# Optimization experiments

Measured on AMD Instinct MI355X. Metric: run time of the kernel, lower is better.

Reference implementation:

```python
import jax, jax.numpy as jnp
import numpy as np

NUM_TAGS = 19
START_ID = 17  # lbl_to_id['START_LBL']
PAD_ID = 18    # lbl_to_id['PAD_LBL']
NEG = -1000.0


def setup_inputs() -> dict:
    key = jax.random.key(0)
    k1, k2, k3 = jax.random.split(key, 3)
    B, L = 512, 2048
    P = jax.random.normal(k1, (B, L, NUM_TAGS), dtype=jnp.float32)
    T = jax.random.normal(k2, (NUM_TAGS, NUM_TAGS), dtype=jnp.float32)
    # contiguous-prefix valid mask, lengths in [1, L]
    lengths = jax.random.randint(k3, (B,), 1, L + 1)
    mask = jnp.arange(L)[None, :] < lengths[:, None]  # [B, L] bool
    return {"P": P, "T": T, "mask": mask}


def _viterbi_forward(P, T, mask):
    # P: [B, L, K] emissions; T[j, k] = score of transition prev=k -> cur=j
    B, L, K = P.shape
    DP0 = jnp.full((B, K), NEG, dtype=P.dtype).at[:, START_ID].set(0.0)

    def step(DP, xs):
        emit, m = xs  # emit: [B, K], m: [B] bool
        scores = DP[:, None, :] + T[None, :, :]        # [B, cur, prev]
        best = scores.max(axis=-1)                      # [B, K]
        arg = scores.argmax(axis=-1).astype(jnp.int32)  # [B, K] backpointers
        new_DP = best + emit
        DP = jnp.where(m[:, None], new_DP, DP)          # frozen past sequence end
        return DP, arg

    DP, choice = jax.lax.scan(
        step, DP0, (jnp.swapaxes(P, 0, 1), jnp.swapaxes(mask, 0, 1))
    )  # choice: [L, B, K]
    DP = DP + T[PAD_ID][None, :]  # transition into PAD at the end
    return DP, choice


def reference(P, T, mask):
    B, L, K = P.shape
    DP, choice = _viterbi_forward(P, T, mask)
    last = DP.argmax(axis=-1).astype(jnp.int32)          # [B] best final tag
    lengths = mask.sum(axis=-1).astype(jnp.int32)        # [B]
    bidx = jnp.arange(B)

    def back(c, t):
        # path[t] = choice[t+1][path[t+1]] for t < len-1; path[len-1] = last
        nxt = choice[jnp.minimum(t + 1, L - 1), bidx, c]  # [B]
        new_c = jnp.where(t < lengths - 1, nxt, c)
        out = jnp.where(t < lengths, new_c, -1)           # -1 pads beyond length
        return new_c, out

    _, outs = jax.lax.scan(back, last, jnp.arange(L - 1, -1, -1))  # [L, B]
    path = jnp.flip(jnp.swapaxes(outs, 0, 1), axis=1)  # [B, L], decoded tags
    return path
```

## Files before the change

### kernel.cpp

```cpp
#include <hip/hip_runtime.h>

#define Bn 512
#define Ln 2048
#define Kn 19
#define NEGV (-1000.0f)
#define START_IDn 17
#define PAD_IDn 18
#define SEG 64
#define PBYTES 79691776u


#define DP_CORE(BASE)                                                          \
    float4 q0 = *(const float4*)((BASE) + 0);                                  \
    float4 q1 = *(const float4*)((BASE) + 4);                                  \
    float4 q2 = *(const float4*)((BASE) + 8);                                  \
    float4 q3 = *(const float4*)((BASE) + 12);                                 \
    float4 q4 = *(const float4*)((BASE) + 16);            \
    float cand[Kn];                                                            \
    cand[0]  = q0.x + Trow[0];  cand[1]  = q0.y + Trow[1];                     \
    cand[2]  = q0.z + Trow[2];  cand[3]  = q0.w + Trow[3];                     \
    cand[4]  = q1.x + Trow[4];  cand[5]  = q1.y + Trow[5];                     \
    cand[6]  = q1.z + Trow[6];  cand[7]  = q1.w + Trow[7];                     \
    cand[8]  = q2.x + Trow[8];  cand[9]  = q2.y + Trow[9];                     \
    cand[10] = q2.z + Trow[10]; cand[11] = q2.w + Trow[11];                    \
    cand[12] = q3.x + Trow[12]; cand[13] = q3.y + Trow[13];                    \
    cand[14] = q3.z + Trow[14]; cand[15] = q3.w + Trow[15];                    \
    cand[16] = q4.x + Trow[16]; cand[17] = q4.y + Trow[17];                    \
    cand[18] = q4.z + Trow[18];                                                \
    float m0 = fmaxf(fmaxf(cand[0],  cand[1]),  cand[2]);                      \
    float m1 = fmaxf(fmaxf(cand[3],  cand[4]),  cand[5]);                      \
    float m2 = fmaxf(fmaxf(cand[6],  cand[7]),  cand[8]);                      \
    float m3 = fmaxf(fmaxf(cand[9],  cand[10]), cand[11]);                     \
    float m4 = fmaxf(fmaxf(cand[12], cand[13]), cand[14]);                     \
    float m5 = fmaxf(fmaxf(cand[15], cand[16]), cand[17]);                     \
    float n0 = fmaxf(fmaxf(m0, m1), m2);                                       \
    float n1 = fmaxf(fmaxf(m3, m4), cand[18]);                                 \
    float best = fmaxf(fmaxf(n0, n1), m5);

__global__ __launch_bounds__(64, 1) void crf_fwd(
    const float* __restrict__ P, const float* __restrict__ T,
    const int* __restrict__ mask, float* __restrict__ dpck,
    float* __restrict__ dpfin, int* __restrict__ lens)
{
    const int lane = threadIdx.x;
    const int half = lane >> 5;
    const int c = lane & 31;
    const int b = blockIdx.x * 2 + half;
    const int cc = (c < Kn) ? c : (Kn - 1);

    float Trow[Kn];
#pragma unroll
    for (int p = 0; p < Kn; ++p) Trow[p] = T[cc * Kn + p];

    const int* mrow = mask + (size_t)b * Ln;
    int sum = 0;
#pragma unroll
    for (int j = 0; j < Ln / 128; ++j) {
        int4 v = *(const int4*)(mrow + j * 128 + c * 4);
        sum += v.x + v.y + v.z + v.w;
    }
#pragma unroll
    for (int k = 1; k < 32; k <<= 1) sum += __shfl_xor(sum, k, 64);
    const int len = sum;
    if (c == 0) lens[b] = len;
    const int lenO = __shfl_xor(len, 32, 64);
    int maxlen = len > lenO ? len : lenO;
    int lmin = len < lenO ? len : lenO;
    lmin = __builtin_amdgcn_readfirstlane(lmin);
    int mlen = (maxlen + (SEG - 1)) & ~(SEG - 1);
    mlen = __builtin_amdgcn_readfirstlane(mlen);

    __shared__ float dp[2][32];
    __shared__ float ebuf[2][2][1280];

    float mydp = (c == START_IDn) ? 0.0f : NEGV;
    dp[half][c] = mydp;

    const unsigned bbyte = (unsigned)b * (Ln * Kn * 4u);
    const unsigned limit = PBYTES - 16;
    const char* Pc = (const char*)P;
    float4 r[10];

#define STAGE_LOAD(ci)                                                         \
    { unsigned base_ = bbyte + (unsigned)(ci) * 4864u + ((unsigned)c << 4);    \
      _Pragma("unroll")                                                        \
      for (int i_ = 0; i_ < 10; ++i_) {                                        \
          unsigned o_ = base_ + (unsigned)i_ * 512u;                           \
          if (o_ > limit) o_ = limit;                                          \
          r[i_] = *(const float4*)(Pc + o_);                                   \
      } }
#define STAGE_WRITE(nb)                                                        \
    { float* d_ = &ebuf[nb][half][(unsigned)c << 2];                           \
      _Pragma("unroll")                                                        \
      for (int i_ = 0; i_ < 10; ++i_) *(float4*)(d_ + i_ * 128) = r[i_]; }

    int buf = 0;
    STAGE_LOAD(0);
    STAGE_WRITE(0);

    for (int t0 = 0; t0 < mlen; t0 += SEG) {
        if (c < Kn)
            dpck[((unsigned)b * 32u + (unsigned)(t0 >> 6)) * (unsigned)Kn + (unsigned)c] = mydp;
        STAGE_LOAD((t0 >> 6) + 1);
        const float* ebl = &ebuf[buf][half][0];

        if (t0 + SEG <= lmin) {
            for (int tt = 0; tt < SEG; tt += 8) {
#pragma unroll
                for (int u = 0; u < 8; ++u) {
                    const float e = ebl[(tt + u) * Kn + cc];
                    const float* base_ = &dp[half][0];
                    DP_CORE(base_)
                    mydp = best + e;
                    dp[half][c] = mydp;
                }
            }
        } else {
            for (int tt = 0; tt < SEG; tt += 8) {
#pragma unroll
                for (int u = 0; u < 8; ++u) {
                    const int t = t0 + tt + u;
                    const float e = ebl[(tt + u) * Kn + cc];
                    const float* base_ = &dp[half][0];
                    DP_CORE(base_)
                    float nd = best + e;
                    mydp = (t < len) ? nd : mydp;
                    dp[half][c] = mydp;
                }
            }
        }
        STAGE_WRITE(buf ^ 1);
        buf ^= 1;
    }
    if (c < Kn) dpfin[b * Kn + c] = mydp;
#undef STAGE_LOAD
#undef STAGE_WRITE
}

__global__ __launch_bounds__(256) void crf_rec(
    const float* __restrict__ P, const float* __restrict__ T,
    const float* __restrict__ dpck, const int* __restrict__ lens,
    unsigned char* __restrict__ choice)
{
    const int tid = threadIdx.x;
    const int halfid = tid >> 5;
    const int c = tid & 31;
    const int cc = (c < Kn) ? c : (Kn - 1);
    const int task = blockIdx.x * 8 + halfid;
    const int b = task >> 5;
    const int seg = task & 31;
    const int t0 = seg * SEG;
    const int len = lens[b];
    if (t0 >= len) return;

    __shared__ float dp[8][32];
    __shared__ __align__(16) unsigned char cbuf[8][SEG * Kn];

    float Trow[Kn];
#pragma unroll
    for (int p = 0; p < Kn; ++p) Trow[p] = T[cc * Kn + p];

    float mydp = (c < Kn) ? dpck[((unsigned)b * 32u + (unsigned)seg) * (unsigned)Kn + (unsigned)c]
                          : NEGV;
    dp[halfid][c] = mydp;

    const float* prow = P + (size_t)b * Ln * Kn + (size_t)t0 * Kn;

    float eb[8];
#pragma unroll
    for (int u = 0; u < 8; ++u) eb[u] = prow[u * Kn + cc];

    for (int tt = 0; tt < SEG; tt += 8) {
#pragma unroll
        for (int u = 0; u < 8; ++u) {
            const int t = t0 + tt + u;
            const float e = eb[u];
            const float* base_ = &dp[halfid][0];
            DP_CORE(base_)
            float nd = best + e;
            mydp = (t < len) ? nd : mydp;
            dp[halfid][c] = mydp;

            int arg = Kn - 1;
#pragma unroll
            for (int p = Kn - 2; p >= 0; --p)
                arg = (cand[p] == best) ? p : arg;
            if (c < Kn) cbuf[halfid][(tt + u) * Kn + c] = (unsigned char)arg;

            int tn = tt + u + 8;
            int tloc = (t0 + tn < Ln) ? tn : (Ln - 1 - t0);
            eb[u] = prow[tloc * Kn + cc];
        }
    }
    {
        const int4* s = (const int4*)&cbuf[halfid][0];
        int4* d = (int4*)(choice + (size_t)b * Ln * Kn + (size_t)t0 * Kn);
        for (int i = c; i < (SEG * Kn) / 16; i += 32) d[i] = s[i];
    }
}

__global__ __launch_bounds__(384, 1) void crf_bwd(
    const float* __restrict__ T, const unsigned char* __restrict__ choice,
    const float* __restrict__ dpfin, const int* __restrict__ lens,
    int* __restrict__ out)
{
    __shared__ unsigned char comp[Ln * Kn];
    __shared__ int vchain[17];
    __shared__ int s_last, s_len;

    const int b = blockIdx.x;
    const int tid = threadIdx.x;

    {
        const int4* src = (const int4*)(choice + (size_t)b * Ln * Kn);
        int4* dst = (int4*)comp;
        for (int i = tid; i < (Ln * Kn) / 16; i += 384) dst[i] = src[i];
    }
    if (tid == 0) {
        s_len = lens[b];
        float bestv = dpfin[b * Kn + 0] + T[PAD_IDn * Kn + 0];
        int bl = 0;
        for (int ci = 1; ci < Kn; ++ci) {
            float v = dpfin[b * Kn + ci] + T[PAD_IDn * Kn + ci];
            if (v > bestv) { bestv = v; bl = ci; }
        }
        s_last = bl;
    }
    __syncthreads();
    const int len = s_len;

    {
        const int wv = tid >> 6;
        const int lane = tid & 63;
        const int ch = wv * 3 + lane / Kn;
        const int c = lane % Kn;
        if (lane < 3 * Kn && ch < 16) {
            int cur = c;
            const int tb = ch * 128 + 127;
            for (int i = 0; i < 128; ++i) {
                const int t = tb - i;
                int nv = comp[t * Kn + cur];
                cur = (t < len) ? nv : cur;
                comp[t * Kn + c] = cur;
            }
        }
    }
    __syncthreads();

    if (tid == 0) {
        int v = s_last;
        vchain[16] = v;
        for (int ch = 15; ch >= 0; --ch) {
            v = comp[ch * 128 * Kn + v];
            vchain[ch] = v;
        }
    }
    __syncthreads();

    const int last = s_last;
    int* orow = out + (size_t)b * Ln;
    for (int t = tid; t < Ln; t += 384) {
        int val;
        if (t >= len) {
            val = -1;
        } else if (t == Ln - 1) {
            val = last;
        } else {
            const int tp = t + 1;
            const int vc = vchain[(tp >> 7) + 1];
            val = comp[tp * Kn + vc];
        }
        orow[t] = val;
    }
}

extern "C" void kernel_launch(void* const* d_in, const int* in_sizes, int n_in,
                              void* d_out, int out_size, void* d_ws, size_t ws_size,
                              hipStream_t stream)
{
    const float* P    = (const float*)d_in[0];
    const float* T    = (const float*)d_in[1];
    const int*   mask = (const int*)d_in[2];
    int* out = (int*)d_out;

    const size_t choice_bytes = (size_t)Bn * Ln * Kn;
    unsigned char* choice = (unsigned char*)d_ws;
    float* dpfin = (float*)((char*)d_ws + choice_bytes);
    int* lens = (int*)((char*)d_ws + choice_bytes + (size_t)Bn * Kn * 4);

    float* dpck = (float*)((char*)d_out + 2 * 1024 * 1024);

    crf_fwd<<<Bn / 2, 64, 0, stream>>>(P, T, mask, dpck, dpfin, lens);
    crf_rec<<<(Bn * 32) / 8, 256, 0, stream>>>(P, T, dpck, lens, choice);
    crf_bwd<<<Bn, 384, 0, stream>>>(T, choice, dpfin, lens, out);
}
```

Before: 400.3 us.

## Use one batch row per wave with readlane DP broadcast in forward pass

Reassigns the forward Viterbi kernel from two rows per wave (half-waves) to one row per wave, doubling the grid. The per-step DP exchange through shared memory is replaced by 19 readlane broadcasts, removing the LDS store/load round trip from the serial dependency chain. Each row now iterates only to its own length instead of the pair's maximum. Trade-off: half the lanes per wave are idle and more waves are launched, and readlane serialization may add its own latency.

```diff
diff --git a/kernel.cpp b/kernel.cpp
--- a/kernel.cpp
+++ b/kernel.cpp
@@ -37,16 +37,32 @@
     float n1 = fmaxf(fmaxf(m3, m4), cand[18]);                                 \
     float best = fmaxf(fmaxf(n0, n1), m5);
 
+#define FWD_CORE()                                                             \
+    float cand[Kn];                                                            \
+    _Pragma("unroll")                                                          \
+    for (int p_ = 0; p_ < Kn; ++p_) {                                          \
+        float s_ = __uint_as_float(                                            \
+            __builtin_amdgcn_readlane(__float_as_uint(mydp), p_));             \
+        cand[p_] = s_ + Trow[p_];                                              \
+    }                                                                          \
+    float m0 = fmaxf(fmaxf(cand[0],  cand[1]),  cand[2]);                      \
+    float m1 = fmaxf(fmaxf(cand[3],  cand[4]),  cand[5]);                      \
+    float m2 = fmaxf(fmaxf(cand[6],  cand[7]),  cand[8]);                      \
+    float m3 = fmaxf(fmaxf(cand[9],  cand[10]), cand[11]);                     \
+    float m4 = fmaxf(fmaxf(cand[12], cand[13]), cand[14]);                     \
+    float m5 = fmaxf(fmaxf(cand[15], cand[16]), cand[17]);                     \
+    float n0 = fmaxf(fmaxf(m0, m1), m2);                                       \
+    float n1 = fmaxf(fmaxf(m3, m4), cand[18]);                                 \
+    float best = fmaxf(fmaxf(n0, n1), m5);
+
 __global__ __launch_bounds__(64, 1) void crf_fwd(
     const float* __restrict__ P, const float* __restrict__ T,
     const int* __restrict__ mask, float* __restrict__ dpck,
     float* __restrict__ dpfin, int* __restrict__ lens)
 {
     const int lane = threadIdx.x;
-    const int half = lane >> 5;
-    const int c = lane & 31;
-    const int b = blockIdx.x * 2 + half;
-    const int cc = (c < Kn) ? c : (Kn - 1);
+    const int b = blockIdx.x;
+    const int cc = (lane < Kn) ? lane : (Kn - 1);
 
     float Trow[Kn];
 #pragma unroll
@@ -55,64 +71,55 @@
     const int* mrow = mask + (size_t)b * Ln;
     int sum = 0;
 #pragma unroll
-    for (int j = 0; j < Ln / 128; ++j) {
-        int4 v = *(const int4*)(mrow + j * 128 + c * 4);
+    for (int j = 0; j < Ln / 256; ++j) {
+        int4 v = *(const int4*)(mrow + j * 256 + lane * 4);
         sum += v.x + v.y + v.z + v.w;
     }
 #pragma unroll
-    for (int k = 1; k < 32; k <<= 1) sum += __shfl_xor(sum, k, 64);
-    const int len = sum;
-    if (c == 0) lens[b] = len;
-    const int lenO = __shfl_xor(len, 32, 64);
-    int maxlen = len > lenO ? len : lenO;
-    int lmin = len < lenO ? len : lenO;
-    lmin = __builtin_amdgcn_readfirstlane(lmin);
-    int mlen = (maxlen + (SEG - 1)) & ~(SEG - 1);
-    mlen = __builtin_amdgcn_readfirstlane(mlen);
-
-    __shared__ float dp[2][32];
-    __shared__ float ebuf[2][2][1280];
-
-    float mydp = (c == START_IDn) ? 0.0f : NEGV;
-    dp[half][c] = mydp;
+    for (int k = 1; k < 64; k <<= 1) sum += __shfl_xor(sum, k, 64);
+    int len = __builtin_amdgcn_readfirstlane(sum);
+    if (lane == 0) lens[b] = len;
+    const int mlen = (len + (SEG - 1)) & ~(SEG - 1);
+
+    __shared__ float ebuf[2][1280];
+
+    float mydp = (lane == START_IDn) ? 0.0f : NEGV;
 
     const unsigned bbyte = (unsigned)b * (Ln * Kn * 4u);
     const unsigned limit = PBYTES - 16;
     const char* Pc = (const char*)P;
-    float4 r[10];
+    float4 r[5];
 
 #define STAGE_LOAD(ci)                                                         \
-    { unsigned base_ = bbyte + (unsigned)(ci) * 4864u + ((unsigned)c << 4);    \
+    { unsigned base_ = bbyte + (unsigned)(ci) * 4864u + ((unsigned)lane << 4); \
       _Pragma("unroll")                                                        \
-      for (int i_ = 0; i_ < 10; ++i_) {                                        \
-          unsigned o_ = base_ + (unsigned)i_ * 512u;                           \
+      for (int i_ = 0; i_ < 5; ++i_) {                                         \
+          unsigned o_ = base_ + (unsigned)i_ * 1024u;                          \
           if (o_ > limit) o_ = limit;                                          \
           r[i_] = *(const float4*)(Pc + o_);                                   \
       } }
 #define STAGE_WRITE(nb)                                                        \
-    { float* d_ = &ebuf[nb][half][(unsigned)c << 2];                           \
+    { float* d_ = &ebuf[nb][(unsigned)lane << 2];                              \
       _Pragma("unroll")                                                        \
-      for (int i_ = 0; i_ < 10; ++i_) *(float4*)(d_ + i_ * 128) = r[i_]; }
+      for (int i_ = 0; i_ < 5; ++i_) *(float4*)(d_ + i_ * 256) = r[i_]; }
 
     int buf = 0;
     STAGE_LOAD(0);
     STAGE_WRITE(0);
 
     for (int t0 = 0; t0 < mlen; t0 += SEG) {
-        if (c < Kn)
-            dpck[((unsigned)b * 32u + (unsigned)(t0 >> 6)) * (unsigned)Kn + (unsigned)c] = mydp;
+        if (lane < Kn)
+            dpck[((unsigned)b * 32u + (unsigned)(t0 >> 6)) * (unsigned)Kn + (unsigned)lane] = mydp;
         STAGE_LOAD((t0 >> 6) + 1);
-        const float* ebl = &ebuf[buf][half][0];
-
-        if (t0 + SEG <= lmin) {
+        const float* ebl = &ebuf[buf][0];
+
+        if (t0 + SEG <= len) {
             for (int tt = 0; tt < SEG; tt += 8) {
 #pragma unroll
                 for (int u = 0; u < 8; ++u) {
                     const float e = ebl[(tt + u) * Kn + cc];
-                    const float* base_ = &dp[half][0];
-                    DP_CORE(base_)
+                    FWD_CORE()
                     mydp = best + e;
-                    dp[half][c] = mydp;
                 }
             }
         } else {
@@ -121,18 +128,16 @@
                 for (int u = 0; u < 8; ++u) {
                     const int t = t0 + tt + u;
                     const float e = ebl[(tt + u) * Kn + cc];
-                    const float* base_ = &dp[half][0];
-                    DP_CORE(base_)
+                    FWD_CORE()
                     float nd = best + e;
                     mydp = (t < len) ? nd : mydp;
-                    dp[half][c] = mydp;
                 }
             }
         }
         STAGE_WRITE(buf ^ 1);
         buf ^= 1;
     }
-    if (c < Kn) dpfin[b * Kn + c] = mydp;
+    if (lane < Kn) dpfin[b * Kn + lane] = mydp;
 #undef STAGE_LOAD
 #undef STAGE_WRITE
 }
@@ -290,7 +295,7 @@
 
     float* dpck = (float*)((char*)d_out + 2 * 1024 * 1024);
 
-    crf_fwd<<<Bn / 2, 64, 0, stream>>>(P, T, mask, dpck, dpfin, lens);
+    crf_fwd<<<Bn, 64, 0, stream>>>(P, T, mask, dpck, dpfin, lens);
     crf_rec<<<(Bn * 32) / 8, 256, 0, stream>>>(P, T, dpck, lens, choice);
     crf_bwd<<<Bn, 384, 0, stream>>>(T, choice, dpfin, lens, out);
 }
```

New measurement: 476.4 us. 1.19x slower.

## Pack four sequences per wave in forward pass using DPP/swizzle cross-lane exchange

Applied to the files above, without the earlier changes.

The forward Viterbi kernel is restructured so each 16-lane group handles one sequence, with every lane owning one primary tag and lanes 0-2 also owning tags 16-18. Previous-step scores are exchanged through DPP row permutes and ds_swizzle instead of an LDS round-trip, and emissions are prefetched straight from global memory into registers eight steps ahead instead of being staged through LDS. This halves the number of forward blocks and shortens the per-step dependency chain. The cost is more instructions per step (two max trees per lane) and scattered, non-vectorized global loads of emissions.

```diff
diff --git a/kernel.cpp b/kernel.cpp
--- a/kernel.cpp
+++ b/kernel.cpp
@@ -37,104 +37,147 @@
     float n1 = fmaxf(fmaxf(m3, m4), cand[18]);                                 \
     float best = fmaxf(fmaxf(n0, n1), m5);
 
+#define DPPF(x, ctrl) (__int_as_float(__builtin_amdgcn_update_dpp(            \
+    __float_as_int(x), __float_as_int(x), (ctrl), 0xF, 0xF, false)))
+#define SWZF(x, off) (__int_as_float(__builtin_amdgcn_ds_swizzle(             \
+    __float_as_int(x), (off))))
+
+#define TREE19(RES, TT, GT)                                                    \
+    {                                                                          \
+      float d0 = v0 + TT[0],  d1 = v1 + TT[1],  d2 = v2 + TT[2];               \
+      float d3 = v3 + TT[3],  d4 = v4 + TT[4],  d5 = v5 + TT[5];               \
+      float d6 = v6 + TT[6],  d7 = v7 + TT[7],  d8 = v8 + TT[8];               \
+      float d9 = v9 + TT[9],  d10 = va + TT[10], d11 = vb + TT[11];            \
+      float d12 = vc + TT[12], d13 = vd + TT[13], d14 = ve + TT[14];           \
+      float d15 = vf + TT[15];                                                 \
+      float e16 = g0 + GT[0], e17 = g1 + GT[1], e18 = g2 + GT[2];              \
+      float m0 = fmaxf(fmaxf(d0, d1), d2);                                     \
+      float m1 = fmaxf(fmaxf(d3, d4), d5);                                     \
+      float m2 = fmaxf(fmaxf(d6, d7), d8);                                     \
+      float m3 = fmaxf(fmaxf(d9, d10), d11);                                   \
+      float m4 = fmaxf(fmaxf(d12, d13), d14);                                  \
+      float m5 = fmaxf(fmaxf(d15, e16), e17);                                  \
+      float n0 = fmaxf(fmaxf(m0, m1), m2);                                     \
+      float n1 = fmaxf(fmaxf(m3, m4), m5);                                     \
+      RES = fmaxf(fmaxf(n0, n1), e18);                                         \
+    }
+
+#define FSTEP(U, MASKED)                                                       \
+  {                                                                            \
+    const int t = t0 + tt + (U);                                               \
+    const float v0 = A;                                                        \
+    const float v1 = DPPF(A, 0xB1);                                            \
+    const float v2 = DPPF(A, 0x4E);                                            \
+    const float v3 = DPPF(A, 0x1B);                                            \
+    const float v7 = DPPF(A, 0x141);                                           \
+    const float v6 = DPPF(v7, 0xB1);                                           \
+    const float v5 = DPPF(v7, 0x4E);                                           \
+    const float v4 = DPPF(v7, 0x1B);                                           \
+    const float vf = DPPF(A, 0x140);                                           \
+    const float ve = DPPF(vf, 0xB1);                                           \
+    const float vd = DPPF(vf, 0x4E);                                           \
+    const float vc = DPPF(vf, 0x1B);                                           \
+    const float v8 = DPPF(vf, 0x141);                                          \
+    const float v9 = DPPF(v8, 0xB1);                                           \
+    const float va = DPPF(v8, 0x4E);                                           \
+    const float vb = DPPF(v8, 0x1B);                                           \
+    float bp, bs;                                                              \
+    TREE19(bp, Tp, Gp)                                                         \
+    TREE19(bs, Ts, Gs)                                                         \
+    const float nd  = bp + eb[(U)];                                            \
+    const float nd2 = bs + eb2[(U)];                                           \
+    if (MASKED) {                                                              \
+      A   = (t < len) ? nd  : A;                                               \
+      sec = (t < len) ? nd2 : sec;                                             \
+    } else {                                                                   \
+      A   = nd;                                                                \
+      sec = nd2;                                                               \
+    }                                                                          \
+    g0 = SWZF(sec, 0x10);                                                      \
+    g1 = SWZF(sec, 0x30);                                                      \
+    g2 = SWZF(sec, 0x50);                                                      \
+    int tn = t + 8;                                                            \
+    tn = (tn < Ln) ? tn : (Ln - 1);                                            \
+    eb[(U)]  = prow[tn * Kn + jr];                                             \
+    eb2[(U)] = prow[tn * Kn + o2];                                             \
+  }
+
 __global__ __launch_bounds__(64, 1) void crf_fwd(
     const float* __restrict__ P, const float* __restrict__ T,
     const int* __restrict__ mask, float* __restrict__ dpck,
     float* __restrict__ dpfin, int* __restrict__ lens)
 {
     const int lane = threadIdx.x;
-    const int half = lane >> 5;
-    const int c = lane & 31;
-    const int b = blockIdx.x * 2 + half;
-    const int cc = (c < Kn) ? c : (Kn - 1);
-
-    float Trow[Kn];
-#pragma unroll
-    for (int p = 0; p < Kn; ++p) Trow[p] = T[cc * Kn + p];
+    const int jr = lane & 15;
+    const int row = lane >> 4;
+    const int b = blockIdx.x * 4 + row;
+    const int o2 = 16 + ((jr < 3) ? jr : 2);
+
+    float Tp[16], Ts[16], Gp[3], Gs[3];
+#pragma unroll
+    for (int m = 0; m < 16; ++m) {
+        Tp[m] = T[jr * Kn + (jr ^ m)];
+        Ts[m] = T[o2 * Kn + (jr ^ m)];
+    }
+#pragma unroll
+    for (int i = 0; i < 3; ++i) {
+        Gp[i] = T[jr * Kn + 16 + i];
+        Gs[i] = T[o2 * Kn + 16 + i];
+    }
 
     const int* mrow = mask + (size_t)b * Ln;
     int sum = 0;
 #pragma unroll
-    for (int j = 0; j < Ln / 128; ++j) {
-        int4 v = *(const int4*)(mrow + j * 128 + c * 4);
+    for (int j2 = 0; j2 < 32; ++j2) {
+        int4 v = *(const int4*)(mrow + j2 * 64 + jr * 4);
         sum += v.x + v.y + v.z + v.w;
     }
-#pragma unroll
-    for (int k = 1; k < 32; k <<= 1) sum += __shfl_xor(sum, k, 64);
+    sum += __shfl_xor(sum, 1, 64);
+    sum += __shfl_xor(sum, 2, 64);
+    sum += __shfl_xor(sum, 4, 64);
+    sum += __shfl_xor(sum, 8, 64);
     const int len = sum;
-    if (c == 0) lens[b] = len;
-    const int lenO = __shfl_xor(len, 32, 64);
-    int maxlen = len > lenO ? len : lenO;
-    int lmin = len < lenO ? len : lenO;
-    lmin = __builtin_amdgcn_readfirstlane(lmin);
-    int mlen = (maxlen + (SEG - 1)) & ~(SEG - 1);
-    mlen = __builtin_amdgcn_readfirstlane(mlen);
-
-    __shared__ float dp[2][32];
-    __shared__ float ebuf[2][2][1280];
-
-    float mydp = (c == START_IDn) ? 0.0f : NEGV;
-    dp[half][c] = mydp;
-
-    const unsigned bbyte = (unsigned)b * (Ln * Kn * 4u);
-    const unsigned limit = PBYTES - 16;
-    const char* Pc = (const char*)P;
-    float4 r[10];
-
-#define STAGE_LOAD(ci)                                                         \
-    { unsigned base_ = bbyte + (unsigned)(ci) * 4864u + ((unsigned)c << 4);    \
-      _Pragma("unroll")                                                        \
-      for (int i_ = 0; i_ < 10; ++i_) {                                        \
-          unsigned o_ = base_ + (unsigned)i_ * 512u;                           \
-          if (o_ > limit) o_ = limit;                                          \
-          r[i_] = *(const float4*)(Pc + o_);                                   \
-      } }
-#define STAGE_WRITE(nb)                                                        \
-    { float* d_ = &ebuf[nb][half][(unsigned)c << 2];                           \
-      _Pragma("unroll")                                                        \
-      for (int i_ = 0; i_ < 10; ++i_) *(float4*)(d_ + i_ * 128) = r[i_]; }
-
-    int buf = 0;
-    STAGE_LOAD(0);
-    STAGE_WRITE(0);
+    if (jr == 0) lens[b] = len;
+    int lx = len, ln_ = len;
+    { int u16a = __shfl_xor(lx, 16, 64); lx = lx > u16a ? lx : u16a;
+      int u16b = __shfl_xor(ln_, 16, 64); ln_ = ln_ < u16b ? ln_ : u16b; }
+    { int u32a = __shfl_xor(lx, 32, 64); lx = lx > u32a ? lx : u32a;
+      int u32b = __shfl_xor(ln_, 32, 64); ln_ = ln_ < u32b ? ln_ : u32b; }
+    const int lmin = __builtin_amdgcn_readfirstlane(ln_);
+    const int mlen = (__builtin_amdgcn_readfirstlane(lx) + (SEG - 1)) & ~(SEG - 1);
+
+    float A = NEGV;
+    float sec = (jr == 1) ? 0.0f : NEGV;
+    float g0 = NEGV, g1 = 0.0f, g2 = NEGV;
+
+    const float* prow = P + (size_t)b * Ln * Kn;
+    float eb[8], eb2[8];
+#pragma unroll
+    for (int u = 0; u < 8; ++u) {
+        eb[u]  = prow[u * Kn + jr];
+        eb2[u] = prow[u * Kn + o2];
+    }
 
     for (int t0 = 0; t0 < mlen; t0 += SEG) {
-        if (c < Kn)
-            dpck[((unsigned)b * 32u + (unsigned)(t0 >> 6)) * (unsigned)Kn + (unsigned)c] = mydp;
-        STAGE_LOAD((t0 >> 6) + 1);
-        const float* ebl = &ebuf[buf][half][0];
-
+        {
+            const unsigned ck = ((unsigned)b * 32u + (unsigned)(t0 >> 6)) * (unsigned)Kn;
+            dpck[ck + (unsigned)jr] = A;
+            if (jr < 3) dpck[ck + 16u + (unsigned)jr] = sec;
+        }
         if (t0 + SEG <= lmin) {
             for (int tt = 0; tt < SEG; tt += 8) {
-#pragma unroll
-                for (int u = 0; u < 8; ++u) {
-                    const float e = ebl[(tt + u) * Kn + cc];
-                    const float* base_ = &dp[half][0];
-                    DP_CORE(base_)
-                    mydp = best + e;
-                    dp[half][c] = mydp;
-                }
+                FSTEP(0, 0) FSTEP(1, 0) FSTEP(2, 0) FSTEP(3, 0)
+                FSTEP(4, 0) FSTEP(5, 0) FSTEP(6, 0) FSTEP(7, 0)
             }
         } else {
             for (int tt = 0; tt < SEG; tt += 8) {
-#pragma unroll
-                for (int u = 0; u < 8; ++u) {
-                    const int t = t0 + tt + u;
-                    const float e = ebl[(tt + u) * Kn + cc];
-                    const float* base_ = &dp[half][0];
-                    DP_CORE(base_)
-                    float nd = best + e;
-                    mydp = (t < len) ? nd : mydp;
-                    dp[half][c] = mydp;
-                }
+                FSTEP(0, 1) FSTEP(1, 1) FSTEP(2, 1) FSTEP(3, 1)
+                FSTEP(4, 1) FSTEP(5, 1) FSTEP(6, 1) FSTEP(7, 1)
             }
         }
-        STAGE_WRITE(buf ^ 1);
-        buf ^= 1;
-    }
-    if (c < Kn) dpfin[b * Kn + c] = mydp;
-#undef STAGE_LOAD
-#undef STAGE_WRITE
+    }
+    dpfin[b * Kn + jr] = A;
+    if (jr < 3) dpfin[b * Kn + 16 + jr] = sec;
 }
 
 __global__ __launch_bounds__(256) void crf_rec(
@@ -290,7 +333,7 @@
 
     float* dpck = (float*)((char*)d_out + 2 * 1024 * 1024);
 
-    crf_fwd<<<Bn / 2, 64, 0, stream>>>(P, T, mask, dpck, dpfin, lens);
+    crf_fwd<<<Bn / 4, 64, 0, stream>>>(P, T, mask, dpck, dpfin, lens);
     crf_rec<<<(Bn * 32) / 8, 256, 0, stream>>>(P, T, dpck, lens, choice);
     crf_bwd<<<Bn, 384, 0, stream>>>(T, choice, dpfin, lens, out);
 }
```

Measured after the change: 624.5 us. +56.0%, slower.

## Fuse forward and recompute kernels with producer-consumer wavefronts in one block

Applied to the files above, without the earlier changes.

Merges the forward max-plus scan kernel and the segment recompute/backpointer kernel into one 192-thread block. One wavefront runs the forward DP for two sequences and publishes per-segment checkpoints through shared memory with a flag. Two consumer wavefronts spin-wait on that flag and recompute backpointers for finished segments while the forward pass continues. This removes the global checkpoint round-trip and a kernel launch, and overlaps backpointer work with the serial forward scan. In exchange, the recompute runs on only 2 wavefronts per pair of sequences instead of a wide separate grid, and the spin-wait adds contention on the forward wavefront.

```diff
diff --git a/kernel.cpp b/kernel.cpp
--- a/kernel.cpp
+++ b/kernel.cpp
@@ -37,49 +37,62 @@
     float n1 = fmaxf(fmaxf(m3, m4), cand[18]);                                 \
     float best = fmaxf(fmaxf(n0, n1), m5);
 
-__global__ __launch_bounds__(64, 1) void crf_fwd(
+__global__ __launch_bounds__(192, 1) void crf_fused(
     const float* __restrict__ P, const float* __restrict__ T,
-    const int* __restrict__ mask, float* __restrict__ dpck,
-    float* __restrict__ dpfin, int* __restrict__ lens)
+    const int* __restrict__ mask, float* __restrict__ dpfin,
+    int* __restrict__ lens, unsigned char* __restrict__ choice)
 {
-    const int lane = threadIdx.x;
-    const int half = lane >> 5;
-    const int c = lane & 31;
-    const int b = blockIdx.x * 2 + half;
-    const int cc = (c < Kn) ? c : (Kn - 1);
-
-    float Trow[Kn];
-#pragma unroll
-    for (int p = 0; p < Kn; ++p) Trow[p] = T[cc * Kn + p];
-
-    const int* mrow = mask + (size_t)b * Ln;
-    int sum = 0;
-#pragma unroll
-    for (int j = 0; j < Ln / 128; ++j) {
-        int4 v = *(const int4*)(mrow + j * 128 + c * 4);
-        sum += v.x + v.y + v.z + v.w;
-    }
-#pragma unroll
-    for (int k = 1; k < 32; k <<= 1) sum += __shfl_xor(sum, k, 64);
-    const int len = sum;
-    if (c == 0) lens[b] = len;
-    const int lenO = __shfl_xor(len, 32, 64);
-    int maxlen = len > lenO ? len : lenO;
-    int lmin = len < lenO ? len : lenO;
-    lmin = __builtin_amdgcn_readfirstlane(lmin);
-    int mlen = (maxlen + (SEG - 1)) & ~(SEG - 1);
-    mlen = __builtin_amdgcn_readfirstlane(mlen);
+    const int tid = threadIdx.x;
+    const int w = tid >> 6;
 
     __shared__ float dp[2][32];
     __shared__ float ebuf[2][2][1280];
-
-    float mydp = (c == START_IDn) ? 0.0f : NEGV;
-    dp[half][c] = mydp;
-
-    const unsigned bbyte = (unsigned)b * (Ln * Kn * 4u);
-    const unsigned limit = PBYTES - 16;
-    const char* Pc = (const char*)P;
-    float4 r[10];
+    __shared__ float ckbuf[2][32][20];
+    __shared__ int   s_len2[2];
+    __shared__ int   seg_done[2];
+    __shared__ float rdp[2][2][32];
+    __shared__ __align__(16) unsigned char rcbuf[2][2][1280];
+
+    if (tid < 2) *(volatile int*)&seg_done[tid] = 0;
+    __syncthreads();
+
+    if (w == 0) {
+        __builtin_amdgcn_s_setprio(1);
+        const int lane = tid;
+        const int half = lane >> 5;
+        const int c = lane & 31;
+        const int b = blockIdx.x * 2 + half;
+        const int cc = (c < Kn) ? c : (Kn - 1);
+
+        float Trow[Kn];
+#pragma unroll
+        for (int p = 0; p < Kn; ++p) Trow[p] = T[cc * Kn + p];
+
+        const int* mrow = mask + (size_t)b * Ln;
+        int sum = 0;
+#pragma unroll
+        for (int j = 0; j < Ln / 128; ++j) {
+            int4 v = *(const int4*)(mrow + j * 128 + c * 4);
+            sum += v.x + v.y + v.z + v.w;
+        }
+#pragma unroll
+        for (int k = 1; k < 32; k <<= 1) sum += __shfl_xor(sum, k, 64);
+        const int len = sum;
+        if (c == 0) { lens[b] = len; s_len2[half] = len; }
+        const int lenO = __shfl_xor(len, 32, 64);
+        int maxlen = len > lenO ? len : lenO;
+        int lmin = len < lenO ? len : lenO;
+        lmin = __builtin_amdgcn_readfirstlane(lmin);
+        int mlen = (maxlen + (SEG - 1)) & ~(SEG - 1);
+        mlen = __builtin_amdgcn_readfirstlane(mlen);
+
+        float mydp = (c == START_IDn) ? 0.0f : NEGV;
+        dp[half][c] = mydp;
+
+        const unsigned bbyte = (unsigned)b * (Ln * Kn * 4u);
+        const unsigned limit = PBYTES - 16;
+        const char* Pc = (const char*)P;
+        float4 r[10];
 
 #define STAGE_LOAD(ci)                                                         \
     { unsigned base_ = bbyte + (unsigned)(ci) * 4864u + ((unsigned)c << 4);    \
@@ -94,108 +107,118 @@
       _Pragma("unroll")                                                        \
       for (int i_ = 0; i_ < 10; ++i_) *(float4*)(d_ + i_ * 128) = r[i_]; }
 
-    int buf = 0;
-    STAGE_LOAD(0);
-    STAGE_WRITE(0);
-
-    for (int t0 = 0; t0 < mlen; t0 += SEG) {
-        if (c < Kn)
-            dpck[((unsigned)b * 32u + (unsigned)(t0 >> 6)) * (unsigned)Kn + (unsigned)c] = mydp;
-        STAGE_LOAD((t0 >> 6) + 1);
-        const float* ebl = &ebuf[buf][half][0];
-
-        if (t0 + SEG <= lmin) {
-            for (int tt = 0; tt < SEG; tt += 8) {
-#pragma unroll
-                for (int u = 0; u < 8; ++u) {
-                    const float e = ebl[(tt + u) * Kn + cc];
-                    const float* base_ = &dp[half][0];
-                    DP_CORE(base_)
-                    mydp = best + e;
-                    dp[half][c] = mydp;
+        int buf = 0;
+        STAGE_LOAD(0);
+        STAGE_WRITE(0);
+
+        for (int t0 = 0; t0 < mlen; t0 += SEG) {
+            if (c < Kn) ckbuf[half][t0 >> 6][c] = mydp;
+            __threadfence_block();
+            __asm__ __volatile__("" ::: "memory");
+            if (c == 0) *(volatile int*)&seg_done[half] = (t0 >> 6) + 1;
+
+            STAGE_LOAD((t0 >> 6) + 1);
+            const float* ebl = &ebuf[buf][half][0];
+
+            if (t0 + SEG <= lmin) {
+                for (int tt = 0; tt < SEG; tt += 8) {
+#pragma unroll
+                    for (int u = 0; u < 8; ++u) {
+                        const float e = ebl[(tt + u) * Kn + cc];
+                        const float* base_ = &dp[half][0];
+                        DP_CORE(base_)
+                        mydp = best + e;
+                        dp[half][c] = mydp;
+                    }
                 }
-            }
-        } else {
-            for (int tt = 0; tt < SEG; tt += 8) {
-#pragma unroll
-                for (int u = 0; u < 8; ++u) {
-                    const int t = t0 + tt + u;
-                    const float e = ebl[(tt + u) * Kn + cc];
-                    const float* base_ = &dp[half][0];
-                    DP_CORE(base_)
-                    float nd = best + e;
-                    mydp = (t < len) ? nd : mydp;
-                    dp[half][c] = mydp;
+            } else {
+                for (int tt = 0; tt < SEG; tt += 8) {
+#pragma unroll
+                    for (int u = 0; u < 8; ++u) {
+                        const int t = t0 + tt + u;
+                        const float e = ebl[(tt + u) * Kn + cc];
+                        const float* base_ = &dp[half][0];
+                        DP_CORE(base_)
+                        float nd = best + e;
+                        mydp = (t < len) ? nd : mydp;
+                        dp[half][c] = mydp;
+                    }
                 }
             }
-        }
-        STAGE_WRITE(buf ^ 1);
-        buf ^= 1;
-    }
-    if (c < Kn) dpfin[b * Kn + c] = mydp;
+            STAGE_WRITE(buf ^ 1);
+            buf ^= 1;
+        }
+        if (c < Kn) dpfin[b * Kn + c] = mydp;
+        __threadfence_block();
+        if (c == 0) *(volatile int*)&seg_done[half] = 32;
 #undef STAGE_LOAD
 #undef STAGE_WRITE
-}
-
-__global__ __launch_bounds__(256) void crf_rec(
-    const float* __restrict__ P, const float* __restrict__ T,
-    const float* __restrict__ dpck, const int* __restrict__ lens,
-    unsigned char* __restrict__ choice)
-{
-    const int tid = threadIdx.x;
-    const int halfid = tid >> 5;
-    const int c = tid & 31;
-    const int cc = (c < Kn) ? c : (Kn - 1);
-    const int task = blockIdx.x * 8 + halfid;
-    const int b = task >> 5;
-    const int seg = task & 31;
-    const int t0 = seg * SEG;
-    const int len = lens[b];
-    if (t0 >= len) return;
-
-    __shared__ float dp[8][32];
-    __shared__ __align__(16) unsigned char cbuf[8][SEG * Kn];
-
-    float Trow[Kn];
-#pragma unroll
-    for (int p = 0; p < Kn; ++p) Trow[p] = T[cc * Kn + p];
-
-    float mydp = (c < Kn) ? dpck[((unsigned)b * 32u + (unsigned)seg) * (unsigned)Kn + (unsigned)c]
-                          : NEGV;
-    dp[halfid][c] = mydp;
-
-    const float* prow = P + (size_t)b * Ln * Kn + (size_t)t0 * Kn;
-
-    float eb[8];
-#pragma unroll
-    for (int u = 0; u < 8; ++u) eb[u] = prow[u * Kn + cc];
-
-    for (int tt = 0; tt < SEG; tt += 8) {
-#pragma unroll
-        for (int u = 0; u < 8; ++u) {
-            const int t = t0 + tt + u;
-            const float e = eb[u];
-            const float* base_ = &dp[halfid][0];
-            DP_CORE(base_)
-            float nd = best + e;
-            mydp = (t < len) ? nd : mydp;
-            dp[halfid][c] = mydp;
-
-            int arg = Kn - 1;
-#pragma unroll
-            for (int p = Kn - 2; p >= 0; --p)
-                arg = (cand[p] == best) ? p : arg;
-            if (c < Kn) cbuf[halfid][(tt + u) * Kn + c] = (unsigned char)arg;
-
-            int tn = tt + u + 8;
-            int tloc = (t0 + tn < Ln) ? tn : (Ln - 1 - t0);
-            eb[u] = prow[tloc * Kn + cc];
-        }
-    }
-    {
-        const int4* s = (const int4*)&cbuf[halfid][0];
-        int4* d = (int4*)(choice + (size_t)b * Ln * Kn + (size_t)t0 * Kn);
-        for (int i = c; i < (SEG * Kn) / 16; i += 32) d[i] = s[i];
+    } else {
+        const int rw = w - 1;
+        const int l = tid & 63;
+        const int rhalf = l >> 5;
+        const int rc = l & 31;
+        const int cc = (rc < Kn) ? rc : (Kn - 1);
+        const int b = blockIdx.x * 2 + rhalf;
+
+        float Trow[Kn];
+#pragma unroll
+        for (int p = 0; p < Kn; ++p) Trow[p] = T[cc * Kn + p];
+
+        const float* pbase = P + (size_t)b * Ln * Kn;
+        int len = Ln + 1;
+
+        for (int s = rw; s < 32; s += 2) {
+            bool need = (s * SEG) < len;
+            if (!__any(need)) break;
+            while (true) {
+                int f = *(volatile int*)&seg_done[rhalf];
+                if (__all((!need) || (f >= s + 1))) break;
+                __builtin_amdgcn_s_sleep(8);
+            }
+            __asm__ __volatile__("" ::: "memory");
+            if (len > Ln) {
+                len = *(volatile int*)&s_len2[rhalf];
+                need = (s * SEG) < len;
+            }
+            if (need) {
+                const int t0 = s * SEG;
+                float mydp = (rc < Kn) ? ckbuf[rhalf][s][rc] : NEGV;
+                rdp[rw][rhalf][rc] = mydp;
+                const float* prow = pbase + (size_t)t0 * Kn;
+
+                float eb[8];
+#pragma unroll
+                for (int u = 0; u < 8; ++u) eb[u] = prow[u * Kn + cc];
+
+                for (int tt = 0; tt < SEG; tt += 8) {
+#pragma unroll
+                    for (int u = 0; u < 8; ++u) {
+                        const int t = t0 + tt + u;
+                        const float e = eb[u];
+                        const float* base_ = &rdp[rw][rhalf][0];
+                        DP_CORE(base_)
+                        float nd = best + e;
+                        mydp = (t < len) ? nd : mydp;
+                        rdp[rw][rhalf][rc] = mydp;
+
+                        int arg = Kn - 1;
+#pragma unroll
+                        for (int p = Kn - 2; p >= 0; --p)
+                            arg = (cand[p] == best) ? p : arg;
+                        if (rc < Kn)
+                            rcbuf[rw][rhalf][(tt + u) * Kn + rc] = (unsigned char)arg;
+
+                        int tn = tt + u + 8;
+                        int tloc = (t0 + tn < Ln) ? tn : (Ln - 1 - t0);
+                        eb[u] = prow[tloc * Kn + cc];
+                    }
+                }
+                const int4* s4 = (const int4*)&rcbuf[rw][rhalf][0];
+                int4* d4 = (int4*)(choice + (size_t)b * Ln * Kn + (size_t)t0 * Kn);
+                for (int i = rc; i < (SEG * Kn) / 16; i += 32) d4[i] = s4[i];
+            }
+        }
     }
 }
 
@@ -288,9 +311,6 @@
     float* dpfin = (float*)((char*)d_ws + choice_bytes);
     int* lens = (int*)((char*)d_ws + choice_bytes + (size_t)Bn * Kn * 4);
 
-    float* dpck = (float*)((char*)d_out + 2 * 1024 * 1024);
-
-    crf_fwd<<<Bn / 2, 64, 0, stream>>>(P, T, mask, dpck, dpfin, lens);
-    crf_rec<<<(Bn * 32) / 8, 256, 0, stream>>>(P, T, dpck, lens, choice);
+    crf_fused<<<Bn / 2, 192, 0, stream>>>(P, T, mask, dpfin, lens, choice);
     crf_bwd<<<Bn, 384, 0, stream>>>(T, choice, dpfin, lens, out);
 }
```

Result: slower. 411.2 us (+2.7%).
